# Kernel tuning notes

Measured on AMD Instinct MI355X. Metric: run time of the kernel, lower is better.

## Reference

```python
import jax, jax.numpy as jnp
import numpy as np
from functools import partial

H = 51  # hidden size hard-coded in the module


def _lstm_cell(x, h, c, W_ih, b_ih, W_hh, b_hh):
    # PyTorch LSTMCell gate order: i, f, g, o stacked along dim 0 of W (4H rows)
    gates = x @ W_ih.T + b_ih + h @ W_hh.T + b_hh  # [B, 4H]
    i, f, g, o = jnp.split(gates, 4, axis=-1)
    i = jax.nn.sigmoid(i)
    f = jax.nn.sigmoid(f)
    g = jnp.tanh(g)
    o = jax.nn.sigmoid(o)
    c_new = f * c + i * g
    h_new = o * jnp.tanh(c_new)
    return h_new, c_new


def setup_inputs() -> dict:
    key = jax.random.key(0)
    ks = jax.random.split(key, 11)
    B, T = 2048, 512
    bound = 1.0 / np.sqrt(H)  # torch LSTMCell/Linear default init: U(-1/sqrt(H), 1/sqrt(H))
    u = lambda k, shape: jax.random.uniform(k, shape, jnp.float32, -bound, bound)
    return {
        "x": jax.random.normal(ks[0], (B, T), dtype=jnp.float32),
        "future": 0,
        "W_ih1": u(ks[1], (4 * H, 1)),
        "b_ih1": u(ks[2], (4 * H,)),
        "W_hh1": u(ks[3], (4 * H, H)),
        "b_hh1": u(ks[4], (4 * H,)),
        "W_ih2": u(ks[5], (4 * H, H)),
        "b_ih2": u(ks[6], (4 * H,)),
        "W_hh2": u(ks[7], (4 * H, H)),
        "b_hh2": u(ks[8], (4 * H,)),
        "fc_w": u(ks[9], (1, H)),
        "fc_b": u(ks[10], (1,)),
    }


def reference(x, future, W_ih1, b_ih1, W_hh1, b_hh1,
              W_ih2, b_ih2, W_hh2, b_hh2, fc_w, fc_b):
    B = x.shape[0]
    z = jnp.zeros((B, H), dtype=x.dtype)

    def cell_stack(x_t, carry):
        h1, c1, h2, c2 = carry
        h1, c1 = _lstm_cell(x_t, h1, c1, W_ih1, b_ih1, W_hh1, b_hh1)
        h2, c2 = _lstm_cell(h1, h2, c2, W_ih2, b_ih2, W_hh2, b_hh2)
        out = h2 @ fc_w.T + fc_b  # [B, 1]
        return (h1, c1, h2, c2), out

    def step(carry, x_t):
        return cell_stack(x_t, carry)

    xs = jnp.swapaxes(x, 0, 1)[:, :, None]  # [T, B, 1]
    carry, outs = jax.lax.scan(step, (z, z, z, z), xs)  # outs: [T, B, 1]
    outputs = jnp.swapaxes(outs[:, :, 0], 0, 1)  # [B, T]

    if future > 0:
        last = outs[-1]  # [B, 1]

        def fstep(c, _):
            inner, out = c
            inner, out = cell_stack(out, inner)
            return (inner, out), out

        _, fouts = jax.lax.scan(fstep, (carry, last), None, length=future)
        outputs = jnp.concatenate([outputs, jnp.swapaxes(fouts[:, :, 0], 0, 1)], axis=1)

    return outputs
```

## Files before the change

kernel.cpp:

```cpp
#include <hip/hip_runtime.h>

#define HID   51
#define T_LEN 512
#define BT    8
#define NTH   512

#define X_OFF   0
#define OUT_OFF 4128
#define H1_OFF  8256
#define H2_OFF  9280

#define L2E 1.4426950408889634f

typedef _Float16 h8 __attribute__((ext_vector_type(8)));
typedef float    f4 __attribute__((ext_vector_type(4)));

__device__ __forceinline__ float fast_rcp(float x) { return __builtin_amdgcn_rcpf(x); }

#if __has_builtin(__builtin_amdgcn_exp2f)
__device__ __forceinline__ float exp2_f(float x) { return __builtin_amdgcn_exp2f(x); }
#else
__device__ __forceinline__ float exp2_f(float x) { return exp2f(x); }
#endif

__device__ __forceinline__ float sigm2(float X) { return fast_rcp(1.0f + exp2_f(-X)); }
__device__ __forceinline__ float tanh2(float E) {
    return fmaf(-2.0f, fast_rcp(exp2_f(E) + 1.0f), 1.0f);
}

__device__ __forceinline__ float dpp_ror8(float v) {
    int t = __builtin_amdgcn_update_dpp(0, __float_as_int(v), 0x128, 0xf, 0xf, true);
    return __int_as_float(t);
}

__device__ __forceinline__ h8 cvt_frag1(const float* p) {
    float4 a = *(const float4*)p;
    float4 b = *(const float4*)(p + 4);
    h8 h;
    h[0] = (_Float16)a.x; h[1] = (_Float16)a.y; h[2] = (_Float16)a.z; h[3] = (_Float16)a.w;
    h[4] = (_Float16)b.x; h[5] = (_Float16)b.y; h[6] = (_Float16)b.z; h[7] = (_Float16)b.w;
    return h;
}

__device__ __forceinline__ h8 h8_zero() {
    h8 z;
    #pragma unroll
    for (int t = 0; t < 8; ++t) z[t] = (_Float16)0.0f;
    return z;
}

__device__ __forceinline__ float gate_update(const float G[4], float& c) {
    float iv = sigm2(G[0]);
    float fv = sigm2(G[1]);
    float gv = tanh2(G[2]);
    float ov = sigm2(G[3]);
    c = fmaf(fv, c, iv * gv);
    return ov * tanh2(c * (2.0f * L2E));
}

#define MFMA16(A, B, C) __builtin_amdgcn_mfma_f32_16x16x32_f16((A), (B), (C), 0, 0, 0)

__global__ __launch_bounds__(NTH)
void lstm_seq_kernel(const float* __restrict__ x,
                     const float* __restrict__ W_ih1, const float* __restrict__ b_ih1,
                     const float* __restrict__ W_hh1, const float* __restrict__ b_hh1,
                     const float* __restrict__ W_ih2, const float* __restrict__ b_ih2,
                     const float* __restrict__ W_hh2, const float* __restrict__ b_hh2,
                     const float* __restrict__ fc_w,  const float* __restrict__ fc_b,
                     float* __restrict__ out)
{
    __shared__ __align__(16) float sb[13312];

    const int tid   = threadIdx.x;
    const int b0    = blockIdx.x * BT;
    const int w     = tid >> 6;
    const int lane  = tid & 63;
    const int row16 = lane & 15;
    const int q4    = lane >> 4;
    const int col   = row16;

    const int  tA   = w;
    const int  tB   = w + 8;
    const bool has2 = (tB < 13);

    h8 a1fA[2], a2fA[4];
    h8 a1fB[2], a2fB[4];

    for (int i = tid; i < 208 * 64; i += NTH) {
        int rp = i >> 6, k = i & 63;
        int j = rp >> 2, g = rp & 3;
        float sc = (g == 2) ? 2.0f * L2E : L2E;
        float v = 0.0f;
        if (j < HID) {
            if (k < HID)           v = W_hh1[(g * HID + j) * HID + k] * sc;
            else if (k == HID)     v = W_ih1[g * HID + j] * sc;
            else if (k == HID + 1) v = (b_ih1[g * HID + j] + b_hh1[g * HID + j]) * sc;
        }
        sb[i] = v;
    }
    __syncthreads();
    #pragma unroll
    for (int kt = 0; kt < 2; ++kt) {
        a1fA[kt] = cvt_frag1(sb + (tA * 16 + row16) * 64 + kt * 32 + q4 * 8);
        a1fB[kt] = has2 ? cvt_frag1(sb + (tB * 16 + row16) * 64 + kt * 32 + q4 * 8)
                        : h8_zero();
    }
    __syncthreads();

    for (int i = tid; i < 208 * 64; i += NTH) {
        int rp = i >> 6, k = i & 63;
        int j = rp >> 2, g = rp & 3;
        float sc = (g == 2) ? 2.0f * L2E : L2E;
        float v = 0.0f;
        if (j < HID) {
            if (k < HID)           v = W_ih2[(g * HID + j) * HID + k] * sc;
            else if (k == HID + 1) v = (b_ih2[g * HID + j] + b_hh2[g * HID + j]) * sc;
        }
        sb[i] = v;
    }
    __syncthreads();
    #pragma unroll
    for (int kt = 0; kt < 2; ++kt) {
        a2fA[kt] = cvt_frag1(sb + (tA * 16 + row16) * 64 + kt * 32 + q4 * 8);
        a2fB[kt] = has2 ? cvt_frag1(sb + (tB * 16 + row16) * 64 + kt * 32 + q4 * 8)
                        : h8_zero();
    }
    __syncthreads();

    for (int i = tid; i < 208 * 64; i += NTH) {
        int rp = i >> 6, k = i & 63;
        int j = rp >> 2, g = rp & 3;
        float sc = (g == 2) ? 2.0f * L2E : L2E;
        float v = 0.0f;
        if (k < HID) {
            if (j < HID)        v = W_hh2[(g * HID + j) * HID + k] * sc;
            else if (rp == 204) v = fc_w[k];
        }
        sb[i] = v;
    }
    __syncthreads();
    #pragma unroll
    for (int kt = 0; kt < 2; ++kt) {
        a2fA[kt + 2] = cvt_frag1(sb + (tA * 16 + row16) * 64 + kt * 32 + q4 * 8);
        a2fB[kt + 2] = has2 ? cvt_frag1(sb + (tB * 16 + row16) * 64 + kt * 32 + q4 * 8)
                            : h8_zero();
    }
    __syncthreads();

    const int jqA = 4 * tA + q4;
    const int jqB = 4 * tB + q4;
    const bool lay1 = (col < 8);
    const int  bsel = col & 7;
    const bool valB = (jqB < HID);
    const int offhA = (lay1 ? H1_OFF : H2_OFF) * 2
                    + (jqA >> 5) * 512 + ((((jqA & 31) >> 3) << 4) + bsel) * 8 + (jqA & 7);
    const int offhB = (lay1 ? H1_OFF : H2_OFF) * 2
                    + (jqB >> 5) * 512 + ((((jqB & 31) >> 3) << 4) + bsel) * 8 + (jqB & 7);
    const bool xwB = (jqB == HID) && lay1;

    float* xl   = sb + X_OFF;
    float* outl = sb + OUT_OFF;
    for (int i = tid; i < BT * 516; i += NTH) {
        int b = i / 516, t = i - 516 * b;
        xl[i] = (t < T_LEN) ? x[(size_t)(b0 + b) * T_LEN + t] : 0.0f;
    }
    for (int i = tid; i < 2048; i += NTH) {
        int w32 = 0;
        if (i < 1024) {
            int r = i & 511;
            int d = r - 386;
            if (d >= 0 && d < 32 && (d & 3) == 0) w32 = 0x00003C00;
        }
        ((int*)(sb + H1_OFF))[i] = w32;
    }

    float cA = 0.f, cB = 0.f;
    const float fcb = fc_b[0];
    const bool outlaneB = (w == 4) && (q4 == 3) && (col < 8);
    const float* xq  = xl + bsel * 516;
    const float* rA0 = sb + H1_OFF + lane * 4;
    const float* rB0 = sb + H2_OFF + lane * 4;
    _Float16* hwpA = (_Float16*)sb + offhA;
    _Float16* hwpB = (_Float16*)sb + offhB;
    const f4 z4 = {0.f, 0.f, 0.f, 0.f};
    __syncthreads();

    if (lay1) {
        {
            float xv = xq[0];
            float G[4];
            #pragma unroll
            for (int g = 0; g < 4; ++g) {
                float sc = (g == 2) ? 2.0f * L2E : L2E;
                float bs = b_ih1[g * HID + jqA] + b_hh1[g * HID + jqA];
                G[g] = sc * fmaf(W_ih1[g * HID + jqA], xv, bs);
            }
            float hv = gate_update(G, cA);
            hwpA[0] = (_Float16)hv;
        }
        if (valB) {
            float xv = xq[0];
            float G[4];
            #pragma unroll
            for (int g = 0; g < 4; ++g) {
                float sc = (g == 2) ? 2.0f * L2E : L2E;
                float bs = b_ih1[g * HID + jqB] + b_hh1[g * HID + jqB];
                G[g] = sc * fmaf(W_ih1[g * HID + jqB], xv, bs);
            }
            float hv = gate_update(G, cB);
            hwpB[0] = (_Float16)hv;
        } else if (xwB) {
            hwpB[0] = (_Float16)xq[1];
        }
    }
    __syncthreads();

    auto body = [&](int i, int p) {
        const float* rA = rA0 + p * 512;
        const float* rB = rB0 + p * 512;
        h8 bh0 = *(const h8*)(rA);       h8 bh1 = *(const h8*)(rA + 256);
        h8 ch2 = *(const h8*)(rB);       h8 ch3 = *(const h8*)(rB + 256);

        if (xwB) hwpB[(p ^ 1) * 1024] = (_Float16)xq[i + 2];

        f4 sA = MFMA16(a1fA[0], bh0, z4);
        f4 sB = MFMA16(a1fB[0], bh0, z4);
        f4 uA = MFMA16(a2fA[0], bh0, z4);
        f4 uB = MFMA16(a2fB[0], bh0, z4);
        sA = MFMA16(a1fA[1], bh1, sA);
        sB = MFMA16(a1fB[1], bh1, sB);
        uA = MFMA16(a2fA[1], bh1, uA);
        uB = MFMA16(a2fB[1], bh1, uB);
        f4 vA = MFMA16(a2fA[2], ch2, z4);
        f4 vB = MFMA16(a2fB[2], ch2, z4);
        vA = MFMA16(a2fA[3], ch3, vA);
        vB = MFMA16(a2fB[3], ch3, vB);
        uA = uA + vA;
        uB = uB + vB;

        {
            float G[4];
            #pragma unroll
            for (int g = 0; g < 4; ++g) {
                float ur = dpp_ror8(uA[g]);
                G[g] = lay1 ? sA[g] : ur;
            }
            float hv = gate_update(G, cA);
            hwpA[(p ^ 1) * 1024] = (_Float16)hv;
        }
        if (has2) {
            float fcv = uB[0];
            float G[4];
            #pragma unroll
            for (int g = 0; g < 4; ++g) {
                float ur = dpp_ror8(uB[g]);
                G[g] = lay1 ? sB[g] : ur;
            }
            float hv = gate_update(G, cB);
            if (valB) hwpB[(p ^ 1) * 1024] = (_Float16)hv;
            if (outlaneB && i >= 1) outl[col * 516 + (i - 1)] = fcb + fcv;
        }
        __syncthreads();
    };
    for (int i = 0; i < T_LEN; i += 2) {
        body(i, 0);
        body(i + 1, 1);
    }
    body(T_LEN, 0);

    for (int i = tid; i < BT * T_LEN; i += NTH) {
        int b = i >> 9, tt = i & (T_LEN - 1);
        out[(size_t)(b0 + b) * T_LEN + tt] = outl[b * 516 + tt];
    }
}

extern "C" void kernel_launch(void* const* d_in, const int* in_sizes, int n_in,
                              void* d_out, int out_size, void* d_ws, size_t ws_size,
                              hipStream_t stream) {
    const float* x      = (const float*)d_in[0];
    const float* W_ih1  = (const float*)d_in[2];
    const float* b_ih1v = (const float*)d_in[3];
    const float* W_hh1  = (const float*)d_in[4];
    const float* b_hh1v = (const float*)d_in[5];
    const float* W_ih2  = (const float*)d_in[6];
    const float* b_ih2v = (const float*)d_in[7];
    const float* W_hh2  = (const float*)d_in[8];
    const float* b_hh2v = (const float*)d_in[9];
    const float* fc_w   = (const float*)d_in[10];
    const float* fc_b   = (const float*)d_in[11];
    float* out = (float*)d_out;

    dim3 grid(2048 / BT);
    dim3 block(NTH);
    lstm_seq_kernel<<<grid, block, 0, stream>>>(x, W_ih1, b_ih1v, W_hh1, b_hh1v,
                                                W_ih2, b_ih2v, W_hh2, b_hh2v,
                                                fc_w, fc_b, out);
}
```

Before: 400.5 us.

## Halve batch tile per block, shrink LDS staging, and fuse gate reciprocals

```diff
diff --git a/kernel.cpp b/kernel.cpp
--- a/kernel.cpp
+++ b/kernel.cpp
@@ -2,13 +2,13 @@
 
 #define HID   51
 #define T_LEN 512
-#define BT    8
+#define BT    4
 #define NTH   512
 
 #define X_OFF   0
-#define OUT_OFF 4128
-#define H1_OFF  8256
-#define H2_OFF  9280
+#define OUT_OFF 2064
+#define H1_OFF  4128
+#define H2_OFF  5152
 
 #define L2E 1.4426950408889634f
 
@@ -22,11 +22,6 @@
 #else
 __device__ __forceinline__ float exp2_f(float x) { return exp2f(x); }
 #endif
-
-__device__ __forceinline__ float sigm2(float X) { return fast_rcp(1.0f + exp2_f(-X)); }
-__device__ __forceinline__ float tanh2(float E) {
-    return fmaf(-2.0f, fast_rcp(exp2_f(E) + 1.0f), 1.0f);
-}
 
 __device__ __forceinline__ float dpp_ror8(float v) {
     int t = __builtin_amdgcn_update_dpp(0, __float_as_int(v), 0x128, 0xf, 0xf, true);
@@ -50,12 +45,15 @@
 }
 
 __device__ __forceinline__ float gate_update(const float G[4], float& c) {
-    float iv = sigm2(G[0]);
-    float fv = sigm2(G[1]);
-    float gv = tanh2(G[2]);
-    float ov = sigm2(G[3]);
-    c = fmaf(fv, c, iv * gv);
-    return ov * tanh2(c * (2.0f * L2E));
+    float ea = exp2_f(-G[0]);
+    float ef = exp2_f(-G[1]);
+    float eg = exp2_f(G[2]);
+    float eo = exp2_f(-G[3]);
+    float fv = fast_rcp(1.0f + ef);
+    float ig = (eg - 1.0f) * fast_rcp((1.0f + ea) * (eg + 1.0f));
+    c = fmaf(fv, c, ig);
+    float ec = exp2_f(fminf(c * (2.0f * L2E), 63.0f));
+    return (ec - 1.0f) * fast_rcp((1.0f + eo) * (ec + 1.0f));
 }
 
 #define MFMA16(A, B, C) __builtin_amdgcn_mfma_f32_16x16x32_f16((A), (B), (C), 0, 0, 0)
@@ -69,7 +67,7 @@
                      const float* __restrict__ fc_w,  const float* __restrict__ fc_b,
                      float* __restrict__ out)
 {
-    __shared__ __align__(16) float sb[13312];
+    __shared__ __align__(16) float sb[7168];
 
     const int tid   = threadIdx.x;
     const int b0    = blockIdx.x * BT;
@@ -86,77 +84,76 @@
     h8 a1fA[2], a2fA[4];
     h8 a1fB[2], a2fB[4];
 
-    for (int i = tid; i < 208 * 64; i += NTH) {
-        int rp = i >> 6, k = i & 63;
+    auto stage_val = [&](int img, int rp, int k) -> float {
         int j = rp >> 2, g = rp & 3;
         float sc = (g == 2) ? 2.0f * L2E : L2E;
         float v = 0.0f;
-        if (j < HID) {
-            if (k < HID)           v = W_hh1[(g * HID + j) * HID + k] * sc;
-            else if (k == HID)     v = W_ih1[g * HID + j] * sc;
-            else if (k == HID + 1) v = (b_ih1[g * HID + j] + b_hh1[g * HID + j]) * sc;
-        }
-        sb[i] = v;
-    }
-    __syncthreads();
-    #pragma unroll
-    for (int kt = 0; kt < 2; ++kt) {
-        a1fA[kt] = cvt_frag1(sb + (tA * 16 + row16) * 64 + kt * 32 + q4 * 8);
-        a1fB[kt] = has2 ? cvt_frag1(sb + (tB * 16 + row16) * 64 + kt * 32 + q4 * 8)
-                        : h8_zero();
-    }
-    __syncthreads();
-
-    for (int i = tid; i < 208 * 64; i += NTH) {
-        int rp = i >> 6, k = i & 63;
-        int j = rp >> 2, g = rp & 3;
-        float sc = (g == 2) ? 2.0f * L2E : L2E;
-        float v = 0.0f;
-        if (j < HID) {
-            if (k < HID)           v = W_ih2[(g * HID + j) * HID + k] * sc;
-            else if (k == HID + 1) v = (b_ih2[g * HID + j] + b_hh2[g * HID + j]) * sc;
-        }
-        sb[i] = v;
-    }
-    __syncthreads();
-    #pragma unroll
-    for (int kt = 0; kt < 2; ++kt) {
-        a2fA[kt] = cvt_frag1(sb + (tA * 16 + row16) * 64 + kt * 32 + q4 * 8);
-        a2fB[kt] = has2 ? cvt_frag1(sb + (tB * 16 + row16) * 64 + kt * 32 + q4 * 8)
-                        : h8_zero();
-    }
-    __syncthreads();
-
-    for (int i = tid; i < 208 * 64; i += NTH) {
-        int rp = i >> 6, k = i & 63;
-        int j = rp >> 2, g = rp & 3;
-        float sc = (g == 2) ? 2.0f * L2E : L2E;
-        float v = 0.0f;
-        if (k < HID) {
-            if (j < HID)        v = W_hh2[(g * HID + j) * HID + k] * sc;
-            else if (rp == 204) v = fc_w[k];
-        }
-        sb[i] = v;
-    }
-    __syncthreads();
-    #pragma unroll
-    for (int kt = 0; kt < 2; ++kt) {
-        a2fA[kt + 2] = cvt_frag1(sb + (tA * 16 + row16) * 64 + kt * 32 + q4 * 8);
-        a2fB[kt + 2] = has2 ? cvt_frag1(sb + (tB * 16 + row16) * 64 + kt * 32 + q4 * 8)
-                            : h8_zero();
-    }
-    __syncthreads();
+        if (img == 0) {
+            if (j < HID) {
+                if (k < HID)           v = W_hh1[(g * HID + j) * HID + k] * sc;
+                else if (k == HID)     v = W_ih1[g * HID + j] * sc;
+                else if (k == HID + 1) v = (b_ih1[g * HID + j] + b_hh1[g * HID + j]) * sc;
+            }
+        } else if (img == 1) {
+            if (j < HID) {
+                if (k < HID)           v = W_ih2[(g * HID + j) * HID + k] * sc;
+                else if (k == HID + 1) v = (b_ih2[g * HID + j] + b_hh2[g * HID + j]) * sc;
+            }
+        } else {
+            if (k < HID) {
+                if (j < HID)        v = W_hh2[(g * HID + j) * HID + k] * sc;
+                else if (rp == 204) v = fc_w[k];
+            }
+        }
+        return v;
+    };
+
+    {
+        const int rlocA_A = (tA * 16 + row16) * 64;
+        const int rlocA_B = ((tA - 7) * 16 + row16) * 64;
+        const int rlocB_B = ((tB - 7) * 16 + row16) * 64;
+        #pragma unroll
+        for (int img = 0; img < 3; ++img) {
+            h8 tA0 = h8_zero(), tA1 = h8_zero();
+            h8 tB0 = h8_zero(), tB1 = h8_zero();
+            for (int i = tid; i < 112 * 64; i += NTH)
+                sb[i] = stage_val(img, i >> 6, i & 63);
+            __syncthreads();
+            if (w <= 6) {
+                tA0 = cvt_frag1(sb + rlocA_A + q4 * 8);
+                tA1 = cvt_frag1(sb + rlocA_A + 32 + q4 * 8);
+            }
+            __syncthreads();
+            for (int i = tid; i < 96 * 64; i += NTH)
+                sb[i] = stage_val(img, 112 + (i >> 6), i & 63);
+            __syncthreads();
+            if (w == 7) {
+                tA0 = cvt_frag1(sb + rlocA_B + q4 * 8);
+                tA1 = cvt_frag1(sb + rlocA_B + 32 + q4 * 8);
+            }
+            if (has2) {
+                tB0 = cvt_frag1(sb + rlocB_B + q4 * 8);
+                tB1 = cvt_frag1(sb + rlocB_B + 32 + q4 * 8);
+            }
+            __syncthreads();
+            if (img == 0)      { a1fA[0] = tA0; a1fA[1] = tA1; a1fB[0] = tB0; a1fB[1] = tB1; }
+            else if (img == 1) { a2fA[0] = tA0; a2fA[1] = tA1; a2fB[0] = tB0; a2fB[1] = tB1; }
+            else               { a2fA[2] = tA0; a2fA[3] = tA1; a2fB[2] = tB0; a2fB[3] = tB1; }
+        }
+    }
 
     const int jqA = 4 * tA + q4;
     const int jqB = 4 * tB + q4;
     const bool lay1 = (col < 8);
-    const int  bsel = col & 7;
-    const bool valB = (jqB < HID);
+    const int  bsel = col & 3;
+    const bool bvalid = ((col & 4) == 0);
+    const bool valA = bvalid;
+    const bool valB = (jqB < HID) && bvalid;
     const int offhA = (lay1 ? H1_OFF : H2_OFF) * 2
                     + (jqA >> 5) * 512 + ((((jqA & 31) >> 3) << 4) + bsel) * 8 + (jqA & 7);
     const int offhB = (lay1 ? H1_OFF : H2_OFF) * 2
                     + (jqB >> 5) * 512 + ((((jqB & 31) >> 3) << 4) + bsel) * 8 + (jqB & 7);
-    const bool xwB = (jqB == HID) && lay1;
+    const bool xwB = (jqB == HID) && lay1 && (col < 4);
 
     float* xl   = sb + X_OFF;
     float* outl = sb + OUT_OFF;
@@ -176,7 +173,7 @@
 
     float cA = 0.f, cB = 0.f;
     const float fcb = fc_b[0];
-    const bool outlaneB = (w == 4) && (q4 == 3) && (col < 8);
+    const bool outlaneB = (w == 4) && (q4 == 3) && (col < 4);
     const float* xq  = xl + bsel * 516;
     const float* rA0 = sb + H1_OFF + lane * 4;
     const float* rB0 = sb + H2_OFF + lane * 4;
@@ -186,7 +183,7 @@
     __syncthreads();
 
     if (lay1) {
-        {
+        if (valA) {
             float xv = xq[0];
             float G[4];
             #pragma unroll
@@ -246,7 +243,7 @@
                 G[g] = lay1 ? sA[g] : ur;
             }
             float hv = gate_update(G, cA);
-            hwpA[(p ^ 1) * 1024] = (_Float16)hv;
+            if (valA) hwpA[(p ^ 1) * 1024] = (_Float16)hv;
         }
         if (has2) {
             float fcv = uB[0];
```

After: 573.8 us. 1.43x slower.
